# Performance work log

Hardware: AMD Instinct MI355X
Metric: run time of the kernel (lower is better)

Reference implementation:

```python
import jax, jax.numpy as jnp
import numpy as np

N_DRUG = 25000
N_DIS = 25000
N = N_DRUG + N_DIS
E = 800000
D_IN = 128
D_OUT = 128


def setup_inputs() -> dict:
    key = jax.random.key(0)
    k1, k2, k3, k4, k5, k6 = jax.random.split(key, 6)
    drug_f = jax.random.normal(k1, (N_DRUG, D_IN), dtype=jnp.float32)
    disease_f = jax.random.normal(k2, (N_DIS, D_IN), dtype=jnp.float32)
    rows = jax.random.randint(k3, (E,), 0, N, dtype=jnp.int64)
    cols = jax.random.randint(k4, (E,), 0, N, dtype=jnp.int64)
    # xavier_uniform_ equivalent for [D_IN, D_OUT]
    limit = float(np.sqrt(6.0 / (D_IN + D_OUT)))
    drug_w = jax.random.uniform(k5, (D_IN, D_OUT), minval=-limit, maxval=limit, dtype=jnp.float32)
    disease_w = jax.random.uniform(k6, (D_IN, D_OUT), minval=-limit, maxval=limit, dtype=jnp.float32)
    return {"drug_f": drug_f, "disease_f": disease_f, "drug_w": drug_w,
            "disease_w": disease_w, "rows": rows, "cols": cols}


def reference(drug_f, disease_f, drug_w, disease_w, rows, cols):
    # per-type linear projection
    drug_h = drug_f @ drug_w          # [n_drug, D_OUT]
    dis_h = disease_f @ disease_w     # [n_dis,  D_OUT]
    node_f = jnp.concatenate([drug_h, dis_h], axis=0)  # [N, D_OUT]
    # row-sum degrees of the (unit-valued) sparse adjacency, clamped at 1
    deg = jax.ops.segment_sum(jnp.ones((rows.shape[0],), node_f.dtype), rows,
                              num_segments=N)
    norm = jnp.clip(deg, 1.0, None) ** -0.5           # [N]
    # symmetric norm: norm * (A @ (norm * x)); SpMM as gather + segment_sum
    node_f = node_f * norm[:, None]
    msgs = node_f[cols]                               # [E, D_OUT]
    node_f = jax.ops.segment_sum(msgs, rows, num_segments=N)
    node_f = node_f * norm[:, None]
    return node_f
```

## Files before the change

kernel.cpp:

```cpp
#include <hip/hip_runtime.h>
#include <hip/hip_bf16.h>

#define D 128
#define CAP 64
#define BINSH 7
#define NSHARD 8
#define NCHUNK 384

typedef short short8 __attribute__((ext_vector_type(8)));
typedef unsigned short ushort8 __attribute__((ext_vector_type(8)));
typedef float f32x4  __attribute__((ext_vector_type(4)));

__device__ __forceinline__ short f2bf(float x) {
    __hip_bfloat16 b = __float2bfloat16(x);
    return *reinterpret_cast<short*>(&b);
}
__device__ __forceinline__ float bf2f(unsigned short u) {
    return __uint_as_float((unsigned)u << 16);
}

__global__ __launch_bounds__(256) void part_proj_kernel(
    const int* __restrict__ rows, const int* __restrict__ cols,
    int* __restrict__ counts, unsigned int* __restrict__ payload,
    int E, int nbin, int nparts, int pe, int capseg,
    const float* __restrict__ f0, const float* __restrict__ f1,
    const float* __restrict__ w0, const float* __restrict__ w1,
    __hip_bfloat16* __restrict__ h,
    int n0, int n1, int nb0) {

    __shared__ short8 Wl[2048];
    int b = blockIdx.x;
    int t = threadIdx.x;

    if (b < nparts) {
        int* cur = (int*)&Wl[0];
        for (int i = t; i < nbin; i += 256) cur[i] = 0;
        __syncthreads();
        int lo = b * pe;
        int hi = lo + pe; if (hi > E) hi = E;
        for (int i = lo + t; i < hi; i += 256) {
            int r = rows[i];
            int c = cols[i];
            int bn = r >> BINSH;
            int p = atomicAdd(&cur[bn], 1);
            if (p < capseg)
                payload[((size_t)bn * nparts + b) * capseg + p] =
                    ((unsigned)r << 16) | (unsigned)(c & 0xffff);
        }
        __syncthreads();
        for (int i = t; i < nbin; i += 256) {
            int c = cur[i]; if (c > capseg) c = capseg;
            counts[(size_t)i * nparts + b] = c;
        }
        return;
    }

    int pb = b - nparts;
    int type = (pb >= nb0) ? 1 : 0;
    const float* f = type ? f1 : f0;
    const float* W = type ? w1 : w0;
    int lbase = (type ? (pb - nb0) : pb) * 64;
    int nloc  = type ? n1 : n0;
    int goff  = type ? n0 : 0;

    for (int i = t; i < 2048; i += 256) {
        int lane = i & 63, ts = i >> 6;
        int s = ts & 3, tt = ts >> 2;
        int n = tt * 16 + (lane & 15);
        int kbase = s * 32 + (lane >> 4) * 8;
        short8 v;
        #pragma unroll
        for (int j = 0; j < 8; ++j)
            v[j] = f2bf(W[(size_t)(kbase + j) * D + n]);
        Wl[i] = v;
    }
    __syncthreads();

    int wave = t >> 6;
    int lane = t & 63;
    int m  = lane & 15;
    int kg = lane >> 4;
    int wrow = lbase + wave * 16;

    int arow = wrow + m;
    int arc = (arow < nloc) ? arow : (nloc - 1);
    const float* fr = f + (size_t)arc * D + kg * 8;
    short8 A[4];
    #pragma unroll
    for (int s = 0; s < 4; ++s) {
        float4 x = *(const float4*)(fr + s * 32);
        float4 y = *(const float4*)(fr + s * 32 + 4);
        short8 a;
        a[0] = f2bf(x.x); a[1] = f2bf(x.y); a[2] = f2bf(x.z); a[3] = f2bf(x.w);
        a[4] = f2bf(y.x); a[5] = f2bf(y.y); a[6] = f2bf(y.z); a[7] = f2bf(y.w);
        A[s] = a;
    }

    #pragma unroll
    for (int tt = 0; tt < 8; ++tt) {
        f32x4 acc = {0.f, 0.f, 0.f, 0.f};
        #pragma unroll
        for (int s = 0; s < 4; ++s)
            acc = __builtin_amdgcn_mfma_f32_16x16x32_bf16(A[s], Wl[(tt * 4 + s) * 64 + lane], acc, 0, 0, 0);
        #pragma unroll
        for (int r = 0; r < 4; ++r) {
            int grow = wrow + kg * 4 + r;
            if (grow < nloc)
                h[(size_t)(goff + grow) * D + tt * 16 + m] = __float2bfloat16(acc[r]);
        }
    }
}

__global__ __launch_bounds__(256) void binfill_kernel(const unsigned int* __restrict__ payload,
                                                      const int* __restrict__ counts,
                                                      unsigned short* __restrict__ bucket,
                                                      int* __restrict__ cnt,
                                                      float* __restrict__ normf,
                                                      int nparts, int capseg, int N) {
    __shared__ int rc[128];
    int b = blockIdx.x;
    int t = threadIdx.x;
    if (t < 128) rc[t] = 0;
    __syncthreads();
    if (t < nparts) {
        int cntc = counts[(size_t)b * nparts + t];
        if (cntc > capseg) cntc = capseg;
        const unsigned int* seg = payload + ((size_t)b * nparts + t) * capseg;
        for (int p = 0; p < cntc; ++p) {
            unsigned pay = seg[p];
            int rl = (pay >> 16) & 127;
            int q = atomicAdd(&rc[rl], 1);
            if (q < CAP)
                bucket[(size_t)((b << BINSH) | rl) * CAP + q] = (unsigned short)(pay & 0xffff);
        }
    }
    __syncthreads();
    if (t < 128) {
        int r = (b << BINSH) | t;
        if (r < N) {
            int c = rc[t];
            cnt[r] = c;
            normf[r] = rsqrtf((float)(c < 1 ? 1 : c));
        }
    }
}

__global__ __launch_bounds__(256) void agg_kernel(const int* __restrict__ cnt,
                                                  const float* __restrict__ normf,
                                                  const unsigned short* __restrict__ bucket,
                                                  const __hip_bfloat16* __restrict__ h,
                                                  float* __restrict__ out, int n) {
    int wave = threadIdx.x >> 6;
    int lane = threadIdx.x & 63;
    int r = blockIdx.x * 4 + wave;
    if (r >= n) return;
    int d = cnt[r]; if (d > CAP) d = CAP;
    int s = r * CAP;

    int col = (int)bucket[s + lane];
    int cs  = (lane < d) ? col : 0;
    float wl = (lane < d) ? normf[cs] : 0.f;

    int g  = lane >> 4;
    int sl = lane & 15;

    float acc[8] = {0.f,0.f,0.f,0.f,0.f,0.f,0.f,0.f};
    int j = 0;
    for (; j + 8 <= d; j += 8) {
        int e0 = j + g, e1 = j + 4 + g;
        float w0 = __shfl(wl, e0);
        float w1 = __shfl(wl, e1);
        int   c0 = __shfl(cs, e0);
        int   c1 = __shfl(cs, e1);
        ushort8 v0 = *(const ushort8*)&h[(size_t)c0 * D + sl * 8];
        ushort8 v1 = *(const ushort8*)&h[(size_t)c1 * D + sl * 8];
        #pragma unroll
        for (int k = 0; k < 8; ++k)
            acc[k] += w0 * bf2f(v0[k]) + w1 * bf2f(v1[k]);
    }
    for (; j < d; j += 4) {
        int e = j + g;
        float we = __shfl(wl, e & 63); if (e >= d) we = 0.f;
        int   ce = __shfl(cs, e & 63);
        ushort8 v = *(const ushort8*)&h[(size_t)ce * D + sl * 8];
        #pragma unroll
        for (int k = 0; k < 8; ++k)
            acc[k] += we * bf2f(v[k]);
    }
    #pragma unroll
    for (int k = 0; k < 8; ++k) {
        acc[k] += __shfl_xor(acc[k], 16);
        acc[k] += __shfl_xor(acc[k], 32);
    }
    if (g == 0) {
        float nr = normf[r];
        float* po = &out[(size_t)r * D + sl * 8];
        *(float4*)po       = make_float4(acc[0]*nr, acc[1]*nr, acc[2]*nr, acc[3]*nr);
        *(float4*)(po + 4) = make_float4(acc[4]*nr, acc[5]*nr, acc[6]*nr, acc[7]*nr);
    }
}

__global__ void zero_cnt_kernel(int* __restrict__ cnt, int N) {
    int i = blockIdx.x * 256 + threadIdx.x;
    if (i < N) cnt[i] = 0;
}

__global__ __launch_bounds__(256) void fill_shard_kernel(const int* __restrict__ rows,
                                                         const int* __restrict__ cols,
                                                         int* __restrict__ cnt,
                                                         unsigned short* __restrict__ bucket,
                                                         int E, int shsz, int ch) {
    int s     = blockIdx.x & (NSHARD - 1);
    int chunk = blockIdx.x >> 3;
    int lo = chunk * ch;
    int hi = lo + ch; if (hi > E) hi = E;
    int rlo = s * shsz;
    for (int i = lo + (int)threadIdx.x; i < hi; i += 256) {
        int r = rows[i];
        if ((unsigned)(r - rlo) < (unsigned)shsz) {
            int p = atomicAdd(&cnt[r], 1);
            if (p < CAP) bucket[(size_t)r * CAP + p] = (unsigned short)cols[i];
        }
    }
}

__global__ void norm_from_cnt_kernel(const int* __restrict__ cnt, float* __restrict__ normf, int N) {
    int i = blockIdx.x * 256 + threadIdx.x;
    if (i < N) { int c = cnt[i]; normf[i] = rsqrtf((float)(c < 1 ? 1 : c)); }
}

extern "C" void kernel_launch(void* const* d_in, const int* in_sizes, int n_in,
                              void* d_out, int out_size, void* d_ws, size_t ws_size,
                              hipStream_t stream) {
    const float* drug_f    = (const float*)d_in[0];
    const float* disease_f = (const float*)d_in[1];
    const float* drug_w    = (const float*)d_in[2];
    const float* disease_w = (const float*)d_in[3];
    const int*   rows      = (const int*)d_in[4];
    const int*   cols      = (const int*)d_in[5];
    float* out = (float*)d_out;

    int n_drug = in_sizes[0] / D;
    int n_dis  = in_sizes[1] / D;
    int N = n_drug + n_dis;
    int E = in_sizes[4];
    (void)out_size; (void)n_in;

    char* ws = (char*)d_ws;
    size_t off = 0;
    auto alloc = [&](size_t bytes) { void* p = ws + off; off = (off + bytes + 255) & ~(size_t)255; return p; };

    int*            cnt      = (int*)alloc(sizeof(int) * N);
    float*          normf    = (float*)alloc(sizeof(float) * N);
    __hip_bfloat16* h_raw    = (__hip_bfloat16*)alloc(sizeof(__hip_bfloat16) * (size_t)N * D);
    unsigned short* bucket   = (unsigned short*)alloc((size_t)N * CAP * sizeof(unsigned short));

    int nb0 = (n_drug + 63) / 64;
    int nb1 = (n_dis + 63) / 64;

    int nbin = (N + (1 << BINSH) - 1) >> BINSH;
    int pe = (E + 255) / 256;
    if (pe < 4096) pe = 4096;
    int nparts = (E + pe - 1) / pe;
    int capseg = ((pe / nbin) * 3 + 31) & ~15;

    size_t sort_need = off
        + ((sizeof(int) * (size_t)nbin * nparts + 255) & ~(size_t)255)
        + ((sizeof(unsigned int) * (size_t)nbin * nparts * capseg + 255) & ~(size_t)255);

    if (ws_size >= sort_need && nbin <= 512 && nparts <= 256) {
        int*          counts  = (int*)alloc(sizeof(int) * (size_t)nbin * nparts);
        unsigned int* payload = (unsigned int*)alloc(sizeof(unsigned int) * (size_t)nbin * nparts * capseg);

        part_proj_kernel<<<nparts + nb0 + nb1, 256, 0, stream>>>(
            rows, cols, counts, payload, E, nbin, nparts, pe, capseg,
            drug_f, disease_f, drug_w, disease_w, h_raw, n_drug, n_dis, nb0);
        binfill_kernel<<<nbin, 256, 0, stream>>>(payload, counts, bucket, cnt, normf,
                                                 nparts, capseg, N);
        agg_kernel<<<(N + 3) / 4, 256, 0, stream>>>(cnt, normf, bucket, h_raw, out, N);
    } else {
        int shsz = (N + NSHARD - 1) / NSHARD;
        int ch   = (E + NCHUNK - 1) / NCHUNK;

        zero_cnt_kernel<<<(N + 255) / 256, 256, 0, stream>>>(cnt, N);
        fill_shard_kernel<<<NCHUNK * NSHARD, 256, 0, stream>>>(rows, cols, cnt, bucket, E, shsz, ch);
        norm_from_cnt_kernel<<<(N + 255) / 256, 256, 0, stream>>>(cnt, normf, N);
        part_proj_kernel<<<nb0 + nb1, 256, 0, stream>>>(
            rows, cols, (int*)nullptr, (unsigned int*)nullptr, E, nbin, 0, pe, capseg,
            drug_f, disease_f, drug_w, disease_w, h_raw, n_drug, n_dis, nb0);
        agg_kernel<<<(N + 3) / 4, 256, 0, stream>>>(cnt, normf, bucket, h_raw, out, N);
    }
}
```

Before: 64.37 us.

## Stage projection output in LDS, flatten binfill loop, unroll gather by 16

```diff
diff --git a/kernel.cpp b/kernel.cpp
--- a/kernel.cpp
+++ b/kernel.cpp
@@ -29,6 +29,7 @@
     int n0, int n1, int nb0) {
 
     __shared__ short8 Wl[2048];
+    __shared__ unsigned short hs[4][16][D];
     int b = blockIdx.x;
     int t = threadIdx.x;
 
@@ -103,10 +104,18 @@
         for (int s = 0; s < 4; ++s)
             acc = __builtin_amdgcn_mfma_f32_16x16x32_bf16(A[s], Wl[(tt * 4 + s) * 64 + lane], acc, 0, 0, 0);
         #pragma unroll
-        for (int r = 0; r < 4; ++r) {
-            int grow = wrow + kg * 4 + r;
-            if (grow < nloc)
-                h[(size_t)(goff + grow) * D + tt * 16 + m] = __float2bfloat16(acc[r]);
+        for (int r = 0; r < 4; ++r)
+            hs[wave][kg * 4 + r][tt * 16 + m] = (unsigned short)f2bf(acc[r]);
+    }
+    int rr = lane >> 4;
+    int ch = lane & 15;
+    #pragma unroll
+    for (int q = 0; q < 4; ++q) {
+        int row = q * 4 + rr;
+        int grow = wrow + row;
+        if (grow < nloc) {
+            ushort8 v = *(const ushort8*)&hs[wave][row][ch * 8];
+            *(ushort8*)&h[(size_t)(goff + grow) * D + ch * 8] = v;
         }
     }
 }
@@ -116,18 +125,25 @@
                                                       unsigned short* __restrict__ bucket,
                                                       int* __restrict__ cnt,
                                                       float* __restrict__ normf,
-                                                      int nparts, int capseg, int N) {
+                                                      int nparts, int capseg_log2, int N) {
     __shared__ int rc[128];
+    __shared__ int ccnt[256];
     int b = blockIdx.x;
     int t = threadIdx.x;
     if (t < 128) rc[t] = 0;
+    int capseg = 1 << capseg_log2;
+    for (int i = t; i < nparts; i += 256) {
+        int c = counts[(size_t)b * nparts + i];
+        ccnt[i] = (c > capseg) ? capseg : c;
+    }
     __syncthreads();
-    if (t < nparts) {
-        int cntc = counts[(size_t)b * nparts + t];
-        if (cntc > capseg) cntc = capseg;
-        const unsigned int* seg = payload + ((size_t)b * nparts + t) * capseg;
-        for (int p = 0; p < cntc; ++p) {
-            unsigned pay = seg[p];
+    const unsigned int* base = payload + ((size_t)b * nparts << capseg_log2);
+    int total = nparts << capseg_log2;
+    for (int i = t; i < total; i += 256) {
+        int chunk = i >> capseg_log2;
+        int p = i & (capseg - 1);
+        if (p < ccnt[chunk]) {
+            unsigned pay = base[i];
             int rl = (pay >> 16) & 127;
             int q = atomicAdd(&rc[rl], 1);
             if (q < CAP)
@@ -166,12 +182,22 @@
 
     float acc[8] = {0.f,0.f,0.f,0.f,0.f,0.f,0.f,0.f};
     int j = 0;
+    for (; j + 16 <= d; j += 16) {
+        int e0 = j + g, e1 = j + 4 + g, e2 = j + 8 + g, e3 = j + 12 + g;
+        float w0 = __shfl(wl, e0), w1 = __shfl(wl, e1), w2 = __shfl(wl, e2), w3 = __shfl(wl, e3);
+        int   c0 = __shfl(cs, e0), c1 = __shfl(cs, e1), c2 = __shfl(cs, e2), c3 = __shfl(cs, e3);
+        ushort8 v0 = *(const ushort8*)&h[(size_t)c0 * D + sl * 8];
+        ushort8 v1 = *(const ushort8*)&h[(size_t)c1 * D + sl * 8];
+        ushort8 v2 = *(const ushort8*)&h[(size_t)c2 * D + sl * 8];
+        ushort8 v3 = *(const ushort8*)&h[(size_t)c3 * D + sl * 8];
+        #pragma unroll
+        for (int k = 0; k < 8; ++k)
+            acc[k] += (w0 * bf2f(v0[k]) + w1 * bf2f(v1[k])) + (w2 * bf2f(v2[k]) + w3 * bf2f(v3[k]));
+    }
     for (; j + 8 <= d; j += 8) {
         int e0 = j + g, e1 = j + 4 + g;
-        float w0 = __shfl(wl, e0);
-        float w1 = __shfl(wl, e1);
-        int   c0 = __shfl(cs, e0);
-        int   c1 = __shfl(cs, e1);
+        float w0 = __shfl(wl, e0), w1 = __shfl(wl, e1);
+        int   c0 = __shfl(cs, e0), c1 = __shfl(cs, e1);
         ushort8 v0 = *(const ushort8*)&h[(size_t)c0 * D + sl * 8];
         ushort8 v1 = *(const ushort8*)&h[(size_t)c1 * D + sl * 8];
         #pragma unroll
@@ -262,21 +288,23 @@
     int pe = (E + 255) / 256;
     if (pe < 4096) pe = 4096;
     int nparts = (E + pe - 1) / pe;
-    int capseg = ((pe / nbin) * 3 + 31) & ~15;
+    int capseg_log2 = 6;
+    while ((1 << capseg_log2) < (pe / nbin) * 3) ++capseg_log2;
+    int capseg = 1 << capseg_log2;
 
     size_t sort_need = off
         + ((sizeof(int) * (size_t)nbin * nparts + 255) & ~(size_t)255)
-        + ((sizeof(unsigned int) * (size_t)nbin * nparts * capseg + 255) & ~(size_t)255);
+        + ((sizeof(unsigned int) * ((size_t)nbin * nparts << capseg_log2) + 255) & ~(size_t)255);
 
     if (ws_size >= sort_need && nbin <= 512 && nparts <= 256) {
         int*          counts  = (int*)alloc(sizeof(int) * (size_t)nbin * nparts);
-        unsigned int* payload = (unsigned int*)alloc(sizeof(unsigned int) * (size_t)nbin * nparts * capseg);
+        unsigned int* payload = (unsigned int*)alloc(sizeof(unsigned int) * ((size_t)nbin * nparts << capseg_log2));
 
         part_proj_kernel<<<nparts + nb0 + nb1, 256, 0, stream>>>(
             rows, cols, counts, payload, E, nbin, nparts, pe, capseg,
             drug_f, disease_f, drug_w, disease_w, h_raw, n_drug, n_dis, nb0);
         binfill_kernel<<<nbin, 256, 0, stream>>>(payload, counts, bucket, cnt, normf,
-                                                 nparts, capseg, N);
+                                                 nparts, capseg_log2, N);
         agg_kernel<<<(N + 3) / 4, 256, 0, stream>>>(cnt, normf, bucket, h_raw, out, N);
     } else {
         int shsz = (N + NSHARD - 1) / NSHARD;
```

New measurement: 75.46 us. 17.2% more time.
